# Performance work log

Measured on AMD Instinct MI355X. Metric: run time of the kernel, lower is better.

The kernel has to match this reference:

```python
import jax, jax.numpy as jnp
import numpy as np

T, B, I, H = 1024, 256, 128, 256

def setup_inputs() -> dict:
    key = jax.random.key(0)
    k1, k2, k3, k4, k5 = jax.random.split(key, 5)
    x = jax.random.normal(k1, (T, B, I), dtype=jnp.float32)
    # nn.Linear default init: U(-1/sqrt(fan_in), 1/sqrt(fan_in))
    sW = 1.0 / np.sqrt(I)
    sV = 1.0 / np.sqrt(H)
    W = jax.random.uniform(k2, (H, I), minval=-sW, maxval=sW, dtype=jnp.float32)
    b_W = jax.random.uniform(k3, (H,), minval=-sW, maxval=sW, dtype=jnp.float32)
    V = jax.random.uniform(k4, (H, H), minval=-sV, maxval=sV, dtype=jnp.float32)
    b_V = jax.random.uniform(k5, (H,), minval=-sV, maxval=sV, dtype=jnp.float32)
    return {"x": x, "W": W, "b_W": b_W, "V": V, "b_V": b_V}

def reference(x, W, b_W, V, b_V):
    # x: (T, B, I). Hidden is always initialized to zeros (as in the torch code).
    # Precompute input projection for all timesteps (same math, one big GEMM).
    xW = jnp.einsum('tbi,hi->tbh', x, W) + b_W  # (T, B, H)
    h0 = jnp.zeros((x.shape[1], V.shape[0]), dtype=x.dtype)

    def step(h, xw_t):
        h_new = jnp.tanh(xw_t + h @ V.T + b_V)
        return h_new, h_new

    h_final, h_seq = jax.lax.scan(step, h0, xW)
    return h_seq, h_final
```

## Files before the change

kernel.cpp:

```cpp
#include <hip/hip_runtime.h>
#include <hip/hip_fp16.h>

#define TT 1024
#define BB 256
#define II 128
#define HH 256

typedef _Float16 f16x8 __attribute__((ext_vector_type(8)));
typedef _Float16 h2    __attribute__((ext_vector_type(2)));
typedef float    f32x4 __attribute__((ext_vector_type(4)));

union HU { h2 h; unsigned u; };
static __device__ __forceinline__ h2 as_h2(unsigned v) { HU t; t.u = v; return t.h; }
static __device__ __forceinline__ unsigned pack2f(float a, float b)
{
    HU t; t.h = h2{(_Float16)a, (_Float16)b}; return t.u;
}

#define LDS_BARRIER()                                            \
    do {                                                         \
        asm volatile("s_waitcnt lgkmcnt(0)" ::: "memory");       \
        __builtin_amdgcn_s_barrier();                            \
        __builtin_amdgcn_sched_barrier(0);                       \
    } while (0)

__device__ __forceinline__ float fast_tanh(float a)
{
    float e = __builtin_amdgcn_exp2f(a * 2.8853900817779268f);
    return 1.0f - 2.0f * __builtin_amdgcn_rcpf(e + 1.0f);
}

static __device__ __forceinline__ f16x8 cvt8(const float* p)
{
    float4 a = *(const float4*)p;
    float4 b = *(const float4*)(p + 4);
    f16x8 r;
    r[0]=(_Float16)a.x; r[1]=(_Float16)a.y; r[2]=(_Float16)a.z; r[3]=(_Float16)a.w;
    r[4]=(_Float16)b.x; r[5]=(_Float16)b.y; r[6]=(_Float16)b.z; r[7]=(_Float16)b.w;
    return r;
}

__global__ __launch_bounds__(256, 1)
void xw_gemm(const float* __restrict__ x, const float* __restrict__ W,
             const float* __restrict__ bW, const float* __restrict__ bV,
             float* __restrict__ xw)
{
    __shared__ _Float16 Wl[HH * II];
    const int tid  = threadIdx.x;
    const int l    = tid & 63;
    const int wv   = (__builtin_amdgcn_readfirstlane(tid) >> 6) & 3;
    const int lr   = l & 15;
    const int kgrp = l >> 4;

    {
        const int row = tid;
        const float4* src = (const float4*)(W + (size_t)row * II);
        unsigned* dst = (unsigned*)Wl;
        const int sw = (row & 7) << 4;
#pragma unroll
        for (int q = 0; q < II / 4; ++q) {
            float4 v = src[q];
            dst[(row * 256 + ((q * 8) ^ sw)) >> 2]     = pack2f(v.x, v.y);
            dst[(row * 256 + ((q * 8 + 4) ^ sw)) >> 2] = pack2f(v.z, v.w);
        }
    }
    __syncthreads();

    const size_t Mbase = (size_t)blockIdx.x * 64;
    const size_t arow  = Mbase + 16 * wv + lr;

    f16x8 afr[4];
#pragma unroll
    for (int kc = 0; kc < 4; ++kc)
        afr[kc] = cvt8(x + arow * II + kc * 32 + kgrp * 8);

    f32x4 acc[16];
#pragma unroll
    for (int nt = 0; nt < 16; ++nt) acc[nt] = f32x4{0.f, 0.f, 0.f, 0.f};

#pragma unroll
    for (int nt = 0; nt < 16; ++nt) {
        const int col = nt * 16 + lr;
        const int sw  = (col & 7) << 4;
#pragma unroll
        for (int kc = 0; kc < 4; ++kc) {
            f16x8 bfr = *(const f16x8*)((const char*)Wl + col * 256 +
                                        ((kc * 64 + kgrp * 16) ^ sw));
            acc[nt] = __builtin_amdgcn_mfma_f32_16x16x32_f16(afr[kc], bfr, acc[nt], 0, 0, 0);
        }
    }
#pragma unroll
    for (int nt = 0; nt < 16; ++nt) {
        const float bias = bW[nt * 16 + lr] + bV[nt * 16 + lr];
#pragma unroll
        for (int r = 0; r < 4; ++r) {
            size_t row = Mbase + 16 * wv + kgrp * 4 + r;
            xw[row * HH + nt * 16 + lr] = acc[nt][r] + bias;
        }
    }
}

__global__ __launch_bounds__(512, 2)
void rnn_v2(const float* __restrict__ V, float* __restrict__ out)
{
    const int b   = blockIdx.x;
    const int tid = threadIdx.x;
    const int l   = tid & 63;
    const int w   = (__builtin_amdgcn_readfirstlane(tid) >> 6) & 7;
    const int lb  = 8 * w;
    const int fo  = 32 * w + (l & 31);
    const bool fact = (l < 32);

    __shared__ __align__(16) _Float16 hbuf[2][HH];
    __shared__ __align__(16) float    pbuf[8][HH];

    h2 Vh[4][16];
#pragma unroll
    for (int c = 0; c < 4; ++c) {
        const int j = 4 * l + c;
        const float* vr = V + (size_t)j * HH + 32 * w;
#pragma unroll
        for (int m = 0; m < 16; ++m)
            Vh[c][m] = h2{(_Float16)vr[2 * m], (_Float16)vr[2 * m + 1]};
    }

    if (tid < HH) { hbuf[0][tid] = (_Float16)0.f; hbuf[1][tid] = (_Float16)0.f; }
    __syncthreads();

    float* __restrict__ seq = out;
    float* __restrict__ fin = out + (size_t)TT * BB * HH;

    float XA = 0.f, XB = 0.f;
    if (fact) {
        XA = seq[((size_t)0 * BB + b) * HH + fo];
        XB = seq[((size_t)1 * BB + b) * HH + fo];
    }

#define RSTEP(P, X, T)                                                          \
    {                                                                           \
        uint2 hv = *(const uint2*)&hbuf[P][4 * l];             \
        h2 a0[4], a1[4];                                                        \
        _Pragma("unroll")                                                       \
        for (int c = 0; c < 4; ++c) { a0[c] = h2{0, 0}; a1[c] = h2{0, 0}; }     \
        _Pragma("unroll")                                                       \
        for (int i2 = 0; i2 < 8; ++i2) {                                        \
            unsigned s0 = (unsigned)__builtin_amdgcn_readlane((int)hv.x, lb + i2); \
            unsigned s1 = (unsigned)__builtin_amdgcn_readlane((int)hv.y, lb + i2); \
            h2 b0 = as_h2(s0), b1 = as_h2(s1);                                  \
            _Pragma("unroll")                                                   \
            for (int c = 0; c < 4; ++c) {                                       \
                a0[c] = __builtin_elementwise_fma(b0, Vh[c][2 * i2],     a0[c]); \
                a1[c] = __builtin_elementwise_fma(b1, Vh[c][2 * i2 + 1], a1[c]); \
            }                                                                   \
        }                                                                       \
        f32x4 tot;                                                              \
        _Pragma("unroll")                                                       \
        for (int c = 0; c < 4; ++c) {                                           \
            h2 s = a0[c] + a1[c];                                               \
            tot[c] = (float)s[0] + (float)s[1];                                 \
        }                                                                       \
        *(f32x4*)&pbuf[w][4 * l] = tot;                                         \
        LDS_BARRIER();                                        \
        if (fact) {                                                             \
            float p0 = pbuf[0][fo], p1 = pbuf[1][fo];                           \
            float p2 = pbuf[2][fo], p3 = pbuf[3][fo];                           \
            float p4 = pbuf[4][fo], p5 = pbuf[5][fo];                           \
            float p6 = pbuf[6][fo], p7 = pbuf[7][fo];                           \
            float r  = (((p0 + p1) + (p2 + p3)) + ((p4 + p5) + (p6 + p7))) + X; \
            float hf = fast_tanh(r);                                            \
            hbuf[(P) ^ 1][fo] = (_Float16)hf;                                   \
            seq[((size_t)(T) * BB + b) * HH + fo] = hf;                         \
            if ((T) == TT - 1) fin[(size_t)b * HH + fo] = hf;                   \
            const int tp = ((T) + 2 < TT) ? (T) + 2 : (TT - 1);                 \
            X = seq[((size_t)tp * BB + b) * HH + fo];                           \
        }                                                                       \
        LDS_BARRIER();                                        \
    }

#pragma unroll 1
    for (int t = 0; t < TT; t += 2) {
        RSTEP(0, XA, t);
        RSTEP(1, XB, t + 1);
    }
#undef RSTEP
}

extern "C" void kernel_launch(void* const* d_in, const int* in_sizes, int n_in,
                              void* d_out, int out_size, void* d_ws, size_t ws_size,
                              hipStream_t stream)
{
    const float* x  = (const float*)d_in[0];
    const float* W  = (const float*)d_in[1];
    const float* bW = (const float*)d_in[2];
    const float* V  = (const float*)d_in[3];
    const float* bV = (const float*)d_in[4];
    float* out = (float*)d_out;

    xw_gemm<<<dim3((TT * BB) / 64), dim3(256), 0, stream>>>(x, W, bW, bV, out);
    rnn_v2<<<dim3(BB), dim3(512), 0, stream>>>(V, out);
}
```

Baseline: 858.2 us.

## Keep hidden state in registers via shuffles and drop one barrier per step

Each wave now produces exactly the 32 hidden values its own V slice consumes. The new h is packed into fp16 pairs in registers with a lane shuffle and broadcast by readlane. The shared-memory hbuf round trip is gone, and the partial-sum buffer is double-buffered, so only one block barrier per timestep is needed instead of two. The inner product also switches from packed fp16 FMAs with fp16 accumulation to fdot2 with fp32 accumulation. This cuts instructions and improves accuracy, but uses round-toward-zero packing for h.

```diff
diff --git a/kernel.cpp b/kernel.cpp
--- a/kernel.cpp
+++ b/kernel.cpp
@@ -8,6 +8,7 @@
 
 typedef _Float16 f16x8 __attribute__((ext_vector_type(8)));
 typedef _Float16 h2    __attribute__((ext_vector_type(2)));
+typedef __fp16   fp16x2 __attribute__((ext_vector_type(2)));
 typedef float    f32x4 __attribute__((ext_vector_type(4)));
 
 union HU { h2 h; unsigned u; };
@@ -15,6 +16,15 @@
 static __device__ __forceinline__ unsigned pack2f(float a, float b)
 {
     HU t; t.h = h2{(_Float16)a, (_Float16)b}; return t.u;
+}
+union PK { fp16x2 h; unsigned u; };
+static __device__ __forceinline__ unsigned pkrtz(float a, float b)
+{
+    PK t; t.h = __builtin_amdgcn_cvt_pkrtz(a, b); return t.u;
+}
+static __device__ __forceinline__ float fdot2u(unsigned a, unsigned b, float c)
+{
+    return __builtin_amdgcn_fdot2(as_h2(a), as_h2(b), c, false);
 }
 
 #define LDS_BARRIER()                                            \
@@ -101,34 +111,31 @@
 }
 
 __global__ __launch_bounds__(512, 2)
-void rnn_v2(const float* __restrict__ V, float* __restrict__ out)
+void rnn_v3(const float* __restrict__ V, float* __restrict__ out)
 {
     const int b   = blockIdx.x;
     const int tid = threadIdx.x;
     const int l   = tid & 63;
     const int w   = (__builtin_amdgcn_readfirstlane(tid) >> 6) & 7;
-    const int lb  = 8 * w;
-    const int fo  = 32 * w + (l & 31);
+    const int j   = l & 31;
+    const int fo  = 32 * w + j;
     const bool fact = (l < 32);
 
-    __shared__ __align__(16) _Float16 hbuf[2][HH];
-    __shared__ __align__(16) float    pbuf[8][HH];
-
-    h2 Vh[4][16];
+    __shared__ __align__(16) float pbuf[2][8][HH];
+
+    unsigned Vh[4][16];
 #pragma unroll
     for (int c = 0; c < 4; ++c) {
-        const int j = 4 * l + c;
-        const float* vr = V + (size_t)j * HH + 32 * w;
-#pragma unroll
-        for (int m = 0; m < 16; ++m)
-            Vh[c][m] = h2{(_Float16)vr[2 * m], (_Float16)vr[2 * m + 1]};
-    }
-
-    if (tid < HH) { hbuf[0][tid] = (_Float16)0.f; hbuf[1][tid] = (_Float16)0.f; }
-    __syncthreads();
+        const int jo = 4 * l + c;
+        const float* vr = V + (size_t)jo * HH + 32 * w;
+#pragma unroll
+        for (int m = 0; m < 16; ++m) Vh[c][m] = pack2f(vr[2 * m], vr[2 * m + 1]);
+    }
 
     float* __restrict__ seq = out;
     float* __restrict__ fin = out + (size_t)TT * BB * HH;
+
+    unsigned pk = 0u;
 
     float XA = 0.f, XB = 0.f;
     if (fact) {
@@ -138,43 +145,35 @@
 
 #define RSTEP(P, X, T)                                                          \
     {                                                                           \
-        uint2 hv = *(const uint2*)&hbuf[P][4 * l];             \
-        h2 a0[4], a1[4];                                                        \
+        float va[4][2] = {{0.f,0.f},{0.f,0.f},{0.f,0.f},{0.f,0.f}};             \
         _Pragma("unroll")                                                       \
-        for (int c = 0; c < 4; ++c) { a0[c] = h2{0, 0}; a1[c] = h2{0, 0}; }     \
-        _Pragma("unroll")                                                       \
-        for (int i2 = 0; i2 < 8; ++i2) {                                        \
-            unsigned s0 = (unsigned)__builtin_amdgcn_readlane((int)hv.x, lb + i2); \
-            unsigned s1 = (unsigned)__builtin_amdgcn_readlane((int)hv.y, lb + i2); \
-            h2 b0 = as_h2(s0), b1 = as_h2(s1);                                  \
+        for (int i = 0; i < 16; ++i) {                                          \
+            unsigned s = (unsigned)__builtin_amdgcn_readlane((int)pk, 2 * i);   \
             _Pragma("unroll")                                                   \
-            for (int c = 0; c < 4; ++c) {                                       \
-                a0[c] = __builtin_elementwise_fma(b0, Vh[c][2 * i2],     a0[c]); \
-                a1[c] = __builtin_elementwise_fma(b1, Vh[c][2 * i2 + 1], a1[c]); \
-            }                                                                   \
+            for (int c = 0; c < 4; ++c)                                         \
+                va[c][i & 1] = fdot2u(s, Vh[c][i], va[c][i & 1]);               \
         }                                                                       \
         f32x4 tot;                                                              \
         _Pragma("unroll")                                                       \
-        for (int c = 0; c < 4; ++c) {                                           \
-            h2 s = a0[c] + a1[c];                                               \
-            tot[c] = (float)s[0] + (float)s[1];                                 \
-        }                                                                       \
-        *(f32x4*)&pbuf[w][4 * l] = tot;                                         \
-        LDS_BARRIER();                                        \
+        for (int c = 0; c < 4; ++c) tot[c] = va[c][0] + va[c][1];               \
+        *(f32x4*)&pbuf[P][w][4 * l] = tot;                                      \
+        LDS_BARRIER();                \
         if (fact) {                                                             \
-            float p0 = pbuf[0][fo], p1 = pbuf[1][fo];                           \
-            float p2 = pbuf[2][fo], p3 = pbuf[3][fo];                           \
-            float p4 = pbuf[4][fo], p5 = pbuf[5][fo];                           \
-            float p6 = pbuf[6][fo], p7 = pbuf[7][fo];                           \
+            float p0 = pbuf[P][0][fo], p1 = pbuf[P][1][fo];                     \
+            float p2 = pbuf[P][2][fo], p3 = pbuf[P][3][fo];                     \
+            float p4 = pbuf[P][4][fo], p5 = pbuf[P][5][fo];                     \
+            float p6 = pbuf[P][6][fo], p7 = pbuf[P][7][fo];                     \
             float r  = (((p0 + p1) + (p2 + p3)) + ((p4 + p5) + (p6 + p7))) + X; \
             float hf = fast_tanh(r);                                            \
-            hbuf[(P) ^ 1][fo] = (_Float16)hf;                                   \
             seq[((size_t)(T) * BB + b) * HH + fo] = hf;                         \
             if ((T) == TT - 1) fin[(size_t)b * HH + fo] = hf;                   \
             const int tp = ((T) + 2 < TT) ? (T) + 2 : (TT - 1);                 \
             X = seq[((size_t)tp * BB + b) * HH + fo];                           \
+            float nb = __shfl_xor(hf, 1, 64);                                   \
+            float lo = (j & 1) ? nb : hf;                                       \
+            float hi = (j & 1) ? hf : nb;                                       \
+            pk = pkrtz(lo, hi);                                                 \
         }                                                                       \
-        LDS_BARRIER();                                        \
     }
 
 #pragma unroll 1
@@ -197,5 +196,5 @@
     float* out = (float*)d_out;
 
     xw_gemm<<<dim3((TT * BB) / 64), dim3(256), 0, stream>>>(x, W, bW, bV, out);
-    rnn_v2<<<dim3(BB), dim3(512), 0, stream>>>(V, out);
-}
+    rnn_v3<<<dim3(BB), dim3(512), 0, stream>>>(V, out);
+}
```

Result: faster. 731.2 us (-14.8%).
